# Performance work log

Measured on AMD Instinct MI355X. Metric: run time of the kernel, lower is better.

The kernel has to match this reference:

```python
import jax, jax.numpy as jnp
import numpy as np

B, DIN, H, DOUT = 8192, 1024, 2048, 1024
P, E = 4, 6            # n_patches, n_edges
C = H // P             # per-patch feature dim = 512
IDX_I = jnp.array([0, 0, 0, 1, 1, 2])  # i<j pair order matches nested loop
IDX_J = jnp.array([1, 2, 3, 2, 3, 3])


def setup_inputs() -> dict:
    key = jax.random.key(0)
    ks = jax.random.split(key, 12)
    s = 0.02
    return {
        "x": jax.random.normal(ks[0], (B, DIN), jnp.float32),
        "fiber": jax.random.normal(ks[1], (B, C), jnp.float32),  # randn_like(base) in torch fwd
        "W_in": jax.random.normal(ks[2], (DIN, H), jnp.float32) * s,
        "b_in": jnp.zeros((H,), jnp.float32),
        "incidence": jax.random.normal(ks[3], (E, P), jnp.float32) * 0.1,
        "sheaf_maps": jnp.tile((jnp.eye(C, dtype=jnp.float32) * 0.1)[None], (E, 1, 1)),
        "damping": jnp.float32(0.1),
        "Wb": jax.random.normal(ks[4], (P, C, C // 2), jnp.float32) * s,
        "bb": jnp.zeros((P, C // 2), jnp.float32),
        "Wf": jax.random.normal(ks[5], (P, C, C // 2), jnp.float32) * s,
        "bf": jnp.zeros((P, C // 2), jnp.float32),
        "Wt": jax.random.normal(ks[6], (C, C), jnp.float32) * s,
        "bt": jnp.zeros((C,), jnp.float32),
        "Wr": jax.random.normal(ks[7], (E, C, C // 2), jnp.float32) * s,
        "br": jnp.zeros((E, C // 2), jnp.float32),
        "Wg": jax.random.normal(ks[8], (H, H), jnp.float32) * s,
        "bg": jnp.zeros((H,), jnp.float32),
        "Wc": jax.random.normal(ks[9], (H + C, DOUT), jnp.float32) * s,
        "bc": jnp.zeros((DOUT,), jnp.float32),
    }


def reference(x, fiber, W_in, b_in, incidence, sheaf_maps, damping,
              Wb, bb, Wf, bf, Wt, bt, Wr, br, Wg, bg, Wc, bc):
    # input projection + split into P contiguous chunks (stack == reshape)
    h = x @ W_in + b_in                                      # [B, H]
    sections = h.reshape(B, P, C)                            # [B, P, C]

    # --- NeuralSheafLaplacian ---
    # coboundary: incidence-weighted combination of patch sections, then per-edge sheaf map
    weighted = jnp.einsum('ep,bpc->bec', incidence, sections)          # [B, E, C]
    coboundary = jnp.einsum('bec,ecd->bed', weighted, sheaf_maps)      # [B, E, C]
    L = incidence.T @ incidence                                        # [P, P] = delta^T delta
    diffused = sections - damping * jnp.einsum('pq,bqc->bpc', L, sections)
    h1_norm = jnp.linalg.norm(coboundary, axis=-1).mean(axis=-1)       # [B]

    # --- FiberBundleLayer ---
    base = diffused.mean(axis=1)                                       # [B, C]
    b_proj = jnp.einsum('bc,scd->bsd', base, Wb) + bb                  # [B, P, C/2]
    f_proj = jnp.einsum('bc,scd->bsd', fiber, Wf) + bf                 # [B, P, C/2]
    simplices = jnp.concatenate([b_proj, f_proj], axis=-1) @ Wt + bt   # [B, P, C]
    total = simplices.mean(axis=1)                                     # [B, C]

    # --- CohomologyConsistency ---
    si = diffused[:, IDX_I]                                            # [B, E, C]
    sj = diffused[:, IDX_J]                                            # [B, E, C]
    ri = jnp.einsum('bec,ecd->bed', si, Wr) + br
    rj = jnp.einsum('bec,ecd->bed', sj, Wr) + br
    h1_loss = jnp.mean((ri - rj) ** 2, axis=(0, 2)).mean()             # mean of per-pair MSEs
    glued = diffused.reshape(B, H) @ Wg + bg                           # cat(sections) == reshape

    output = jnp.concatenate([glued, total], axis=-1) @ Wc + bc        # [B, DOUT]
    return output, diffused, h1_norm, h1_loss, total
```

## Files before the change

### kernel.cpp

```cpp
#include <hip/hip_runtime.h>
#include <cstdint>

#define B_    8192
#define DIN_  1024
#define H_    2048
#define DOUT_ 1024
#define P4_   4
#define E6_   6
#define C_    512
#define C2_   256

typedef __bf16 bf16x8 __attribute__((ext_vector_type(8)));
typedef float  f32x4  __attribute__((ext_vector_type(4)));

__device__ __forceinline__ unsigned short f2bf_bits(float f) {
    unsigned u = __float_as_uint(f);
    unsigned r = (u + 0x7fffu + ((u >> 16) & 1u)) >> 16;
    return (unsigned short)r;
}
__device__ __forceinline__ float bf2f(unsigned short s) {
    return __uint_as_float(((unsigned)s) << 16);
}

__device__ __forceinline__ void async_load16(void* lds, const void* g) {
    __builtin_amdgcn_global_load_lds(
        (__attribute__((address_space(1))) void*)(uintptr_t)g,
        (__attribute__((address_space(3))) void*)(unsigned int)(uintptr_t)lds,
        16, 0, 0);
}


__global__ void convert_f32_bf16_k(const float* __restrict__ in,
                                   unsigned short* __restrict__ out, int n) {
    int i = (blockIdx.x * blockDim.x + threadIdx.x) * 4;
    if (i + 3 < n) {
        float4 v = *(const float4*)(in + i);
        ushort4 o;
        o.x = f2bf_bits(v.x); o.y = f2bf_bits(v.y);
        o.z = f2bf_bits(v.z); o.w = f2bf_bits(v.w);
        *(ushort4*)(out + i) = o;
    }
}

__global__ void convert_fiber_k(const float* __restrict__ in,
                                unsigned short* __restrict__ out) {
    int idx4 = (blockIdx.x * 256 + threadIdx.x) * 4;
    int b = idx4 >> 9, c = idx4 & 511;
    float4 v = *(const float4*)(in + idx4);
    ushort4 o;
    o.x = f2bf_bits(v.x); o.y = f2bf_bits(v.y);
    o.z = f2bf_bits(v.z); o.w = f2bf_bits(v.w);
    *(ushort4*)(out + (long)b * 1024 + 512 + c) = o;
}

__global__ void transpose_to_bf16_k(const float* __restrict__ in,
                                    unsigned short* __restrict__ out,
                                    int R, int Cc, long inStrideZ, long outStrideZ) {
    __shared__ float t[32][33];
    in  += (long)blockIdx.z * inStrideZ;
    out += (long)blockIdx.z * outStrideZ;
    int x0 = blockIdx.x << 5, y0 = blockIdx.y << 5;
    int tx = threadIdx.x, ty = threadIdx.y;
#pragma unroll
    for (int j = 0; j < 32; j += 8)
        t[ty + j][tx] = in[(long)(y0 + ty + j) * Cc + x0 + tx];
    __syncthreads();
#pragma unroll
    for (int j = 0; j < 32; j += 8)
        out[(long)(x0 + ty + j) * R + y0 + tx] = f2bf_bits(t[tx][ty + j]);
}

__global__ void wbar_k(const float* __restrict__ W, unsigned short* __restrict__ out) {
    int id = blockIdx.x * blockDim.x + threadIdx.x;
    float s = 0.f;
#pragma unroll
    for (int si = 0; si < 4; si++) s += W[si * (512 * 256) + id];
    out[id] = f2bf_bits(0.25f * s);
}

__global__ void bbar_k(const float* __restrict__ b, float* __restrict__ out) {
    int d = threadIdx.x;
    out[d] = 0.25f * (b[d] + b[256 + d] + b[512 + d] + b[768 + d]);
}

__global__ void btot_k(const float* __restrict__ bbar, const float* __restrict__ bfbar,
                       const float* __restrict__ Wt, const float* __restrict__ bt,
                       float* __restrict__ btot) {
    int n = blockIdx.x * 256 + threadIdx.x;
    float s = bt[n];
#pragma unroll 4
    for (int d = 0; d < 256; d++)
        s += bbar[d] * Wt[d * 512 + n] + bfbar[d] * Wt[(256 + d) * 512 + n];
    btot[n] = s;
}

__global__ void copy_wc_tail_k(const unsigned short* __restrict__ src,
                               unsigned short* __restrict__ dst) {
    int id = blockIdx.x * 256 + threadIdx.x;
    int n = id >> 7, c4 = (id & 127) << 2;
    long off = (long)n * 2560 + 2048 + c4;
    *(ushort4*)(dst + off) = *(const ushort4*)(src + off);
}

__global__ void bout_k(const float* __restrict__ bg, const float* __restrict__ Wc,
                       const float* __restrict__ bc, float* __restrict__ bout) {
    int n = blockIdx.x * 256 + threadIdx.x;
    int j0 = blockIdx.y << 7;
    float s = (blockIdx.y == 0) ? bc[n] : 0.f;
#pragma unroll 4
    for (int j = 0; j < 128; j++) s += bg[j0 + j] * Wc[(long)(j0 + j) * 1024 + n];
    atomicAdd(&bout[n], s);
}

__global__ void k2_diffuse_k(const unsigned short* __restrict__ hb,
                             const float* __restrict__ incidence,
                             const float* __restrict__ damping,
                             float* __restrict__ outDiff,
                             unsigned short* __restrict__ diffb,
                             unsigned short* __restrict__ basefib,
                             unsigned short* __restrict__ weightedb,
                             unsigned short* __restrict__ debuf) {
    __shared__ float M4[4][4];
    __shared__ float inc2[24];
    int tid = threadIdx.x;
    if (tid < 16) {
        int p = tid >> 2, q = tid & 3;
        float l = 0.f;
#pragma unroll
        for (int e = 0; e < 6; e++) l += incidence[e * 4 + p] * incidence[e * 4 + q];
        M4[p][q] = (p == q ? 1.f : 0.f) - damping[0] * l;
    }
    if (tid < 24) inc2[tid] = incidence[tid];
    __syncthreads();

    int b = blockIdx.x >> 1;
    int c = ((blockIdx.x & 1) << 8) + tid;
    long hoff = (long)b * H_ + c;
    long doff = (long)b * 2560 + c;
    float s0 = bf2f(hb[hoff]);
    float s1 = bf2f(hb[hoff + 512]);
    float s2 = bf2f(hb[hoff + 1024]);
    float s3 = bf2f(hb[hoff + 1536]);

    float d0 = M4[0][0]*s0 + M4[0][1]*s1 + M4[0][2]*s2 + M4[0][3]*s3;
    float d1 = M4[1][0]*s0 + M4[1][1]*s1 + M4[1][2]*s2 + M4[1][3]*s3;
    float d2 = M4[2][0]*s0 + M4[2][1]*s1 + M4[2][2]*s2 + M4[2][3]*s3;
    float d3 = M4[3][0]*s0 + M4[3][1]*s1 + M4[3][2]*s2 + M4[3][3]*s3;

    outDiff[hoff]        = d0;
    outDiff[hoff + 512]  = d1;
    outDiff[hoff + 1024] = d2;
    outDiff[hoff + 1536] = d3;
    diffb[doff]        = f2bf_bits(d0);
    diffb[doff + 512]  = f2bf_bits(d1);
    diffb[doff + 1024] = f2bf_bits(d2);
    diffb[doff + 1536] = f2bf_bits(d3);
    basefib[(long)b * 1024 + c] = f2bf_bits(0.25f * (d0 + d1 + d2 + d3));

#pragma unroll
    for (int e = 0; e < 6; e++) {
        float w = inc2[e*4+0]*s0 + inc2[e*4+1]*s1 + inc2[e*4+2]*s2 + inc2[e*4+3]*s3;
        weightedb[(long)e * (B_ * (long)C_) + (long)b * C_ + c] = f2bf_bits(w);
    }
    float dI[6] = {d0, d0, d0, d1, d1, d2};
    float dJ[6] = {d1, d2, d3, d2, d3, d3};
#pragma unroll
    for (int e = 0; e < 6; e++)
        debuf[(long)e * (B_ * (long)C_) + (long)b * C_ + c] = f2bf_bits(dI[e] - dJ[e]);
}

template <int MODE>
__global__ __launch_bounds__(256, 2)
void gemm_bt_k(const unsigned short* __restrict__ A, long sAz, int lda,
               const unsigned short* __restrict__ Bt, long sBz, int ldb, int K,
               const float* __restrict__ bias,
               unsigned short* __restrict__ Cb, int ldcb,
               float* __restrict__ Cf, int ldcf, long sCz,
               float* __restrict__ red, long sRz) {
    __shared__ __align__(16) unsigned short smA[128 * 64];
    __shared__ __align__(16) unsigned short smB[128 * 64];
    const int tid = threadIdx.x;
    const int lane = tid & 63, w = tid >> 6;
    const int wm = w >> 1, wn = w & 1;
    const int m16 = lane & 15, quad = lane >> 4;
    const int m7 = m16 & 7;

    const int nwg = gridDim.x * gridDim.y;
    const int bid = blockIdx.y * gridDim.x + blockIdx.x;
    const int lid = (nwg & 7) ? bid : (((bid & 7) * (nwg >> 3)) + (bid >> 3));
    const int bx = lid % gridDim.x;
    const int by = lid / gridDim.x;

    A  += (long)blockIdx.z * sAz;
    Bt += (long)blockIdx.z * sBz;
    const long rowA0 = (long)by * 128;
    const long rowB0 = (long)bx * 128;

    f32x4 acc[4][4];
#pragma unroll
    for (int i = 0; i < 4; i++)
#pragma unroll
        for (int j = 0; j < 4; j++) acc[i][j] = f32x4{0.f, 0.f, 0.f, 0.f};

    for (int k0 = 0; k0 < K; k0 += 64) {
#pragma unroll
        for (int i = 0; i < 4; i++) {
            int chunk = i * 256 + tid;
            int row = chunk >> 3;
            int keS = ((chunk & 7) ^ (row & 7)) << 3;
            async_load16(&smA[chunk << 3], A  + (rowA0 + row) * (long)lda + k0 + keS);
            async_load16(&smB[chunk << 3], Bt + (rowB0 + row) * (long)ldb + k0 + keS);
        }
        __syncthreads();
#pragma unroll
        for (int kk = 0; kk < 64; kk += 32) {
            const int pc = (((kk >> 3) + quad) ^ m7) << 3;
            bf16x8 af[4], bfv[4];
#pragma unroll
            for (int i = 0; i < 4; i++) {
                af[i]  = *(const bf16x8*)&smA[((wm << 6) + (i << 4) + m16) * 64 + pc];
                bfv[i] = *(const bf16x8*)&smB[((wn << 6) + (i << 4) + m16) * 64 + pc];
            }
#pragma unroll
            for (int i = 0; i < 4; i++)
#pragma unroll
                for (int j = 0; j < 4; j++)
                    acc[i][j] = __builtin_amdgcn_mfma_f32_16x16x32_bf16(af[i], bfv[j], acc[i][j], 0, 0, 0);
        }
        __syncthreads();
    }

    const long rowBase = rowA0 + (wm << 6);
    const long colBase = rowB0 + (wn << 6);

    if (MODE <= 2) {
        Cb += (long)blockIdx.z * sCz;
        Cf += (long)blockIdx.z * sCz;
#pragma unroll
        for (int j = 0; j < 4; j++) {
            long col = colBase + (j << 4) + m16;
            float bv = bias ? bias[col] : 0.f;
#pragma unroll
            for (int i = 0; i < 4; i++) {
                long row = rowBase + (i << 4) + (quad << 2);
#pragma unroll
                for (int r = 0; r < 4; r++) {
                    float v = acc[i][j][r] + bv;
                    if (MODE == 0 || MODE == 2) Cb[(row + r) * (long)ldcb + col] = f2bf_bits(v);
                    if (MODE == 1 || MODE == 2) Cf[(row + r) * (long)ldcf + col] = v;
                }
            }
        }
    } else if (MODE == 3) {
        float* rz = red + (long)blockIdx.z * sRz;
#pragma unroll
        for (int i = 0; i < 4; i++) {
            float v0 = 0.f, v1 = 0.f, v2 = 0.f, v3 = 0.f;
#pragma unroll
            for (int j = 0; j < 4; j++) {
                float a0 = acc[i][j][0], a1 = acc[i][j][1], a2 = acc[i][j][2], a3 = acc[i][j][3];
                v0 += a0 * a0; v1 += a1 * a1; v2 += a2 * a2; v3 += a3 * a3;
            }
#pragma unroll
            for (int m = 1; m <= 8; m <<= 1) {
                v0 += __shfl_xor(v0, m); v1 += __shfl_xor(v1, m);
                v2 += __shfl_xor(v2, m); v3 += __shfl_xor(v3, m);
            }
            if (m16 == 0) {
                long row = rowBase + (i << 4) + (quad << 2);
                atomicAdd(&rz[row + 0], v0);
                atomicAdd(&rz[row + 1], v1);
                atomicAdd(&rz[row + 2], v2);
                atomicAdd(&rz[row + 3], v3);
            }
        }
    } else {
        float s = 0.f;
#pragma unroll
        for (int i = 0; i < 4; i++)
#pragma unroll
            for (int j = 0; j < 4; j++)
#pragma unroll
                for (int r = 0; r < 4; r++) { float a = acc[i][j][r]; s += a * a; }
#pragma unroll
        for (int m = 1; m <= 32; m <<= 1) s += __shfl_xor(s, m);
        if (lane == 0) atomicAdd(red, s);
    }
}

__global__ void f1_h1norm_k(const float* __restrict__ hn, float* __restrict__ out) {
    int b = blockIdx.x * 256 + threadIdx.x;
    float s = 0.f;
#pragma unroll
    for (int e = 0; e < 6; e++) s += sqrtf(hn[e * B_ + b]);
    out[b] = s * (1.f / 6.f);
}

__global__ void f2_h1loss_k(const float* __restrict__ acc, float* __restrict__ out) {
    if (threadIdx.x == 0) out[0] = acc[0] * (1.f / (8192.f * 6.f * 256.f));
}

extern "C" void kernel_launch(void* const* d_in, const int* in_sizes, int n_in,
                              void* d_out, int out_size, void* d_ws, size_t ws_size,
                              hipStream_t stream) {
    const float* x     = (const float*)d_in[0];
    const float* fiber = (const float*)d_in[1];
    const float* W_in  = (const float*)d_in[2];
    const float* b_in  = (const float*)d_in[3];
    const float* incid = (const float*)d_in[4];
    const float* sheaf = (const float*)d_in[5];
    const float* damp  = (const float*)d_in[6];
    const float* Wb    = (const float*)d_in[7];
    const float* bb    = (const float*)d_in[8];
    const float* Wf    = (const float*)d_in[9];
    const float* bfv   = (const float*)d_in[10];
    const float* Wt    = (const float*)d_in[11];
    const float* bt    = (const float*)d_in[12];
    const float* Wr    = (const float*)d_in[13];
    const float* Wg    = (const float*)d_in[15];
    const float* bg    = (const float*)d_in[16];
    const float* Wc    = (const float*)d_in[17];
    const float* bc    = (const float*)d_in[18];

    float* out      = (float*)d_out;
    float* outDiff  = out + 8388608;
    float* outH1n   = out + 25165824;
    float* outH1l   = out + 25174016;
    float* outTotal = out + 25174017;

    char* ws = (char*)d_ws;
    size_t o = 0;
    auto alloc = [&](size_t bytes) { size_t r = o; o += (bytes + 255) & ~(size_t)255; return r; };

    size_t r0 = alloc(50331648);
    unsigned short* xb = (unsigned short*)(ws + r0);
    unsigned short* hb = (unsigned short*)(ws + r0 + 16777216);
    unsigned short* Ab2560    = (unsigned short*)(ws + alloc(41943040));
    unsigned short* basefibb  = (unsigned short*)(ws + alloc(16777216));
    unsigned short* weightedb = (unsigned short*)(ws + alloc(50331648));
    unsigned short* debuf     = (unsigned short*)(ws + alloc(50331648));
    unsigned short* WinT   = (unsigned short*)(ws + alloc(4194304));
    unsigned short* Wgb    = (unsigned short*)(ws + alloc(8388608));
    unsigned short* WcT    = (unsigned short*)(ws + alloc(5242880));
    unsigned short* WoutT  = (unsigned short*)(ws + alloc(5242880));
    unsigned short* WtT    = (unsigned short*)(ws + alloc(524288));
    unsigned short* WrT    = (unsigned short*)(ws + alloc(1572864));
    unsigned short* ShT    = (unsigned short*)(ws + alloc(3145728));
    unsigned short* WbarCat= (unsigned short*)(ws + alloc(524288));
    unsigned short* WcombT = (unsigned short*)(ws + alloc(1048576));
    float* bbarf  = (float*)(ws + alloc(1024));
    float* bfbarf = (float*)(ws + alloc(1024));
    float* btotf  = (float*)(ws + alloc(2048));
    float* boutf  = (float*)(ws + alloc(4096));
    float* hnacc  = (float*)(ws + alloc(6 * 8192 * 4 + 256));
    float* lossacc = hnacc + 6 * 8192;

    (void)hipMemsetAsync(hnacc, 0, 6 * 8192 * 4 + 256, stream);
    (void)hipMemsetAsync(boutf, 0, 4096, stream);

    convert_f32_bf16_k<<<8192, 256, 0, stream>>>(x, xb, 8388608);
    convert_fiber_k<<<4096, 256, 0, stream>>>(fiber, basefibb);
    convert_f32_bf16_k<<<4096, 256, 0, stream>>>(Wg, Wgb, 4194304);
    dim3 tb(32, 8);
    transpose_to_bf16_k<<<dim3(64, 32), tb, 0, stream>>>(W_in, WinT, 1024, 2048, 0, 0);
    transpose_to_bf16_k<<<dim3(32, 80), tb, 0, stream>>>(Wc, WcT, 2560, 1024, 0, 0);
    transpose_to_bf16_k<<<dim3(16, 16), tb, 0, stream>>>(Wt, WtT, 512, 512, 0, 0);
    transpose_to_bf16_k<<<dim3(16, 16, 6), tb, 0, stream>>>(sheaf, ShT, 512, 512, 512 * 512, 512 * 512);
    transpose_to_bf16_k<<<dim3(8, 16, 6), tb, 0, stream>>>(Wr, WrT, 512, 256, 512 * 256, 512 * 256);
    wbar_k<<<512, 256, 0, stream>>>(Wb, WbarCat);
    wbar_k<<<512, 256, 0, stream>>>(Wf, WbarCat + 131072);
    bbar_k<<<1, 256, 0, stream>>>(bb, bbarf);
    bbar_k<<<1, 256, 0, stream>>>(bfv, bfbarf);
    btot_k<<<2, 256, 0, stream>>>(bbarf, bfbarf, Wt, bt, btotf);

    gemm_bt_k<0><<<dim3(4, 4, 2), 256, 0, stream>>>(WtT, 256, 512, WbarCat, 131072, 256, 256,
                                                    nullptr, WcombT, 1024, nullptr, 0, 512, nullptr, 0);
    gemm_bt_k<0><<<dim3(16, 8, 1), 256, 0, stream>>>(WcT, 0, 2560, Wgb, 0, 2048, 2048,
                                                     nullptr, WoutT, 2560, nullptr, 0, 0, nullptr, 0);
    copy_wc_tail_k<<<512, 256, 0, stream>>>(WcT, WoutT);
    bout_k<<<dim3(4, 16), 256, 0, stream>>>(bg, Wc, bc, boutf);

    gemm_bt_k<0><<<dim3(16, 64, 1), 256, 0, stream>>>(xb, 0, DIN_, WinT, 0, DIN_, DIN_,
                                                      b_in, hb, H_, nullptr, 0, 0, nullptr, 0);
    k2_diffuse_k<<<16384, 256, 0, stream>>>(hb, incid, damp, outDiff, Ab2560, basefibb, weightedb, debuf);

    gemm_bt_k<3><<<dim3(4, 64, 6), 256, 0, stream>>>(weightedb, (long)B_ * C_, C_, ShT, (long)C_ * C_, C_, C_,
                                                     nullptr, nullptr, 0, nullptr, 0, 0, hnacc, B_);
    gemm_bt_k<4><<<dim3(2, 64, 6), 256, 0, stream>>>(debuf, (long)B_ * C_, C_, WrT, (long)C2_ * C_, C_, C_,
                                                     nullptr, nullptr, 0, nullptr, 0, 0, lossacc, 0);
    gemm_bt_k<2><<<dim3(4, 64, 1), 256, 0, stream>>>(basefibb, 0, 1024, WcombT, 0, 1024, 1024,
                                                     btotf, Ab2560 + 2048, 2560, outTotal, C_, 0, nullptr, 0);
    gemm_bt_k<1><<<dim3(8, 64, 1), 256, 0, stream>>>(Ab2560, 0, 2560, WoutT, 0, 2560, 2560,
                                                     boutf, nullptr, 0, out, DOUT_, 0, nullptr, 0);
    f1_h1norm_k<<<32, 256, 0, stream>>>(hnacc, outH1n);
    f2_h1loss_k<<<1, 64, 0, stream>>>(lossacc, outH1l);

    (void)in_sizes; (void)n_in; (void)out_size; (void)ws_size;
}
```

Measured before the change: 592.4 us.

## Add 256x256-tile 8-wave bf16 GEMM with quarter-staged double buffering for input projection

```diff
diff --git a/kernel.cpp b/kernel.cpp
--- a/kernel.cpp
+++ b/kernel.cpp
@@ -285,6 +285,135 @@
 #pragma unroll
         for (int m = 1; m <= 32; m <<= 1) s += __shfl_xor(s, m);
         if (lane == 0) atomicAdd(red, s);
+    }
+}
+
+__device__ __forceinline__ void stage_quarter(unsigned short* ldsT, const unsigned short* g,
+                                              long ld, int k0, int isB, int qi, int tid) {
+#pragma unroll
+    for (int l = 0; l < 2; ++l) {
+        int c = l * 512 + tid;
+        int i = c >> 3, kc = c & 7;
+        int lr = isB ? (((i >> 5) << 6) + (i & 31) + (qi << 5))
+                     : (((i >> 6) << 7) + (i & 63) + (qi << 6));
+        async_load16(ldsT + lr * 64 + kc * 8,
+                     g + (long)lr * ld + k0 + (((kc ^ (lr & 7))) << 3));
+    }
+}
+
+template <int MODE>
+__global__ __launch_bounds__(512, 2)
+void gemm256_k(const unsigned short* __restrict__ A, int lda,
+               const unsigned short* __restrict__ Bt, int ldb, int K,
+               const float* __restrict__ bias,
+               unsigned short* __restrict__ Cb, float* __restrict__ Cf, int ldc) {
+    extern __shared__ unsigned short sm[];
+    unsigned short* smA = sm;
+    unsigned short* smB = sm + 2 * 16384;
+    const int tid = threadIdx.x;
+    const int lane = tid & 63;
+    const int wid = tid >> 6;
+    const int wm = wid >> 2, wn = wid & 3;
+    const int m16 = lane & 15, quad = lane >> 4;
+    const int m7 = m16 & 7;
+
+    const int nwg = gridDim.x * gridDim.y;
+    const int bid = blockIdx.y * gridDim.x + blockIdx.x;
+    const int lid = (nwg & 7) ? bid : (((bid & 7) * (nwg >> 3)) + (bid >> 3));
+    const int bx = lid % gridDim.x, by = lid / gridDim.x;
+    const long rowA0 = (long)by * 256, rowB0 = (long)bx * 256;
+
+    const unsigned short* gA = A + rowA0 * (long)lda;
+    const unsigned short* gB = Bt + rowB0 * (long)ldb;
+    const int NT = K >> 6;
+
+    f32x4 acc[8][4];
+#pragma unroll
+    for (int i = 0; i < 8; i++)
+#pragma unroll
+        for (int j = 0; j < 4; j++) acc[i][j] = f32x4{0.f, 0.f, 0.f, 0.f};
+
+    stage_quarter(smA,         gA, lda, 0, 0, 0, tid);
+    stage_quarter(smB,         gB, ldb, 0, 1, 0, tid);
+    stage_quarter(smA,         gA, lda, 0, 0, 1, tid);
+    stage_quarter(smB,         gB, ldb, 0, 1, 1, tid);
+    if (NT > 1) {
+        stage_quarter(smA + 16384, gA, lda, 64, 0, 0, tid);
+        stage_quarter(smB + 16384, gB, ldb, 64, 1, 0, tid);
+        asm volatile("s_waitcnt vmcnt(4)" ::: "memory");
+    } else {
+        asm volatile("s_waitcnt vmcnt(0)" ::: "memory");
+    }
+    __builtin_amdgcn_s_barrier();
+
+    for (int t = 0; t < NT; ++t) {
+        const int cur = t & 1;
+        unsigned short* cA = smA + cur * 16384;
+        unsigned short* cB = smB + cur * 16384;
+        unsigned short* nA = smA + (cur ^ 1) * 16384;
+        unsigned short* nB = smB + (cur ^ 1) * 16384;
+        bf16x8 av[4][2];
+#pragma unroll
+        for (int q = 0; q < 4; ++q) {
+            const int mh = q >> 1, nh = q & 1;
+            if (nh == 0) {
+#pragma unroll
+                for (int fi = 0; fi < 4; ++fi)
+#pragma unroll
+                    for (int kk = 0; kk < 2; ++kk)
+                        av[fi][kk] = *(const bf16x8*)&cA[(wm * 128 + mh * 64 + fi * 16 + m16) * 64
+                                                        + ((((kk << 2) + quad)) ^ m7) * 8];
+            }
+            bf16x8 bv[2][2];
+#pragma unroll
+            for (int fj = 0; fj < 2; ++fj)
+#pragma unroll
+                for (int kk = 0; kk < 2; ++kk)
+                    bv[fj][kk] = *(const bf16x8*)&cB[(wn * 64 + nh * 32 + fj * 16 + m16) * 64
+                                                    + ((((kk << 2) + quad)) ^ m7) * 8];
+            if (q == 0) {
+                if (t + 1 < NT) stage_quarter(nB, gB, ldb, (t + 1) << 6, 1, 1, tid);
+            } else if (q == 1) {
+                if (t + 1 < NT) stage_quarter(nA, gA, lda, (t + 1) << 6, 0, 1, tid);
+            } else if (q == 2) {
+                if (t + 2 < NT) stage_quarter(cA, gA, lda, (t + 2) << 6, 0, 0, tid);
+            } else {
+                if (t + 2 < NT) stage_quarter(cB, gB, ldb, (t + 2) << 6, 1, 0, tid);
+                if (t + 2 < NT)      asm volatile("s_waitcnt vmcnt(4)" ::: "memory");
+                else if (t + 1 < NT) asm volatile("s_waitcnt vmcnt(0)" ::: "memory");
+            }
+            __builtin_amdgcn_s_barrier();
+            asm volatile("s_waitcnt lgkmcnt(0)" ::: "memory");
+            __builtin_amdgcn_sched_barrier(0);
+            __builtin_amdgcn_s_setprio(1);
+#pragma unroll
+            for (int fi = 0; fi < 4; ++fi)
+#pragma unroll
+                for (int fj = 0; fj < 2; ++fj)
+#pragma unroll
+                    for (int kk = 0; kk < 2; ++kk)
+                        acc[mh * 4 + fi][nh * 2 + fj] =
+                            __builtin_amdgcn_mfma_f32_16x16x32_bf16(av[fi][kk], bv[fj][kk],
+                                                                    acc[mh * 4 + fi][nh * 2 + fj], 0, 0, 0);
+            __builtin_amdgcn_s_setprio(0);
+            __builtin_amdgcn_s_barrier();
+        }
+    }
+
+#pragma unroll
+    for (int fj = 0; fj < 4; ++fj) {
+        long col = rowB0 + wn * 64 + fj * 16 + m16;
+        float bv2 = bias ? bias[col] : 0.f;
+#pragma unroll
+        for (int mi = 0; mi < 8; ++mi) {
+            long row = rowA0 + wm * 128 + mi * 16 + (quad << 2);
+#pragma unroll
+            for (int r = 0; r < 4; ++r) {
+                float v = acc[mi][fj][r] + bv2;
+                if (MODE == 0) Cb[(row + r) * (long)ldc + col] = f2bf_bits(v);
+                else           Cf[(row + r) * (long)ldc + col] = v;
+            }
+        }
     }
 }
 
@@ -327,6 +456,15 @@
     float* outH1n   = out + 25165824;
     float* outH1l   = out + 25174016;
     float* outTotal = out + 25174017;
+
+    static bool s_attr = false;
+    if (!s_attr) {
+        (void)hipFuncSetAttribute(reinterpret_cast<const void*>(&gemm256_k<0>),
+                                  hipFuncAttributeMaxDynamicSharedMemorySize, 131072);
+        (void)hipFuncSetAttribute(reinterpret_cast<const void*>(&gemm256_k<1>),
+                                  hipFuncAttributeMaxDynamicSharedMemorySize, 131072);
+        s_attr = true;
+    }
 
     char* ws = (char*)d_ws;
     size_t o = 0;
@@ -380,8 +518,8 @@
     copy_wc_tail_k<<<512, 256, 0, stream>>>(WcT, WoutT);
     bout_k<<<dim3(4, 16), 256, 0, stream>>>(bg, Wc, bc, boutf);
 
-    gemm_bt_k<0><<<dim3(16, 64, 1), 256, 0, stream>>>(xb, 0, DIN_, WinT, 0, DIN_, DIN_,
-                                                      b_in, hb, H_, nullptr, 0, 0, nullptr, 0);
+    gemm256_k<0><<<dim3(8, 32), 512, 131072, stream>>>(xb, DIN_, WinT, DIN_, DIN_,
+                                                       b_in, hb, nullptr, H_);
     k2_diffuse_k<<<16384, 256, 0, stream>>>(hb, incid, damp, outDiff, Ab2560, basefibb, weightedb, debuf);
 
     gemm_bt_k<3><<<dim3(4, 64, 6), 256, 0, stream>>>(weightedb, (long)B_ * C_, C_, ShT, (long)C_ * C_, C_, C_,
```

Result: slower. 604.5 us (+2.0%).
